# Optimization experiments

Measured on AMD Instinct MI355X. Metric: run time of the kernel, lower is better.

Reference implementation:

```python
import jax, jax.numpy as jnp
import numpy as np
import math

H, B, T = 4, 32, 1000
EPROJS, DUNITS, DK, DV = 1024, 1024, 512, 512
ACONV_CHANS, ACONV_FILTS = 100, 100
FILTS = [ACONV_FILTS * (h + 1) // H for h in range(H)]  # 25, 50, 75, 100


def setup_inputs() -> dict:
    key = jax.random.key(0)
    ks = jax.random.split(key, 16)
    s = 0.02  # small init to keep tanh unsaturated
    ap = jax.random.uniform(ks[3], (H, B, T), dtype=jnp.float32)
    ap = ap / ap.sum(-1, keepdims=True)  # previous attention weights (rows sum to 1)
    inp = {
        "enc_hs_pad": jax.random.normal(ks[0], (B, T, EPROJS), dtype=jnp.float32),
        "enc_hs_len": jnp.full((B,), T, dtype=jnp.int32),
        "dec_z": jax.random.normal(ks[1], (B, DUNITS), dtype=jnp.float32),
        "att_prev": ap,
        "Wq": jax.random.normal(ks[4], (H, DUNITS, DK), dtype=jnp.float32) * s,
        "bq": jnp.zeros((H, DK), dtype=jnp.float32),
        "Wk": jax.random.normal(ks[5], (H, EPROJS, DK), dtype=jnp.float32) * s,
        "Wv": jax.random.normal(ks[6], (H, EPROJS, DV), dtype=jnp.float32) * s,
        "g_w": jax.random.normal(ks[7], (H, DK), dtype=jnp.float32) * s,
        "g_b": jnp.zeros((H,), dtype=jnp.float32),
        "Watt": jax.random.normal(ks[8], (H, ACONV_CHANS, DK), dtype=jnp.float32) * s,
        "Wo": jax.random.normal(ks[9], (H * DV, EPROJS), dtype=jnp.float32) * s,
    }
    for h in range(H):
        inp[f"conv_w{h}"] = jax.random.normal(ks[10 + h], (ACONV_CHANS, 1, 2 * FILTS[h] + 1), dtype=jnp.float32) * s
    return inp


def _conv1d(x, w, f):
    # x: [B, T], w: [C, 1, K]; SAME padding like torch Conv2d(padding=(0, f)) -> [B, C, T]
    return jax.lax.conv_general_dilated(x[:, None, :], w, (1,), [(f, f)],
                                        dimension_numbers=("NCH", "OIH", "NCH"))


def reference(enc_hs_pad, enc_hs_len, dec_z, att_prev, Wq, bq, Wk, Wv, g_w, g_b,
              Watt, Wo, conv_w0, conv_w1, conv_w2, conv_w3):
    scaling = 1.0 / math.sqrt(DK)
    conv_ws = [conv_w0, conv_w1, conv_w2, conv_w3]
    # per-head K/V projections of encoder states: [H, B, T, dk/dv]
    k = jnp.einsum('btd,hde->hbte', enc_hs_pad, Wk)
    v = jnp.einsum('btd,hde->hbte', enc_hs_pad, Wv)
    # per-head query projection: [H, B, dk]
    q = jnp.einsum('bd,hde->hbe', dec_z, Wq) + bq[:, None, :]
    # location features: per-head conv (different filter widths) then linear -> [H, B, T, dk]
    att_conv = jnp.stack([_conv1d(att_prev[h], conv_ws[h], FILTS[h]).transpose(0, 2, 1)
                          for h in range(H)])  # [H, B, T, C]
    att_conv = jnp.einsum('hbtc,hce->hbte', att_conv, Watt)
    # energies via gvec: [H, B, T]
    e = jnp.einsum('hbte,he->hbt', jnp.tanh(k + att_conv + q[:, :, None, :]), g_w) + g_b[:, None, None]
    w = jax.nn.softmax(scaling * e, axis=-1)  # no length masking, as in the original
    # weighted sums per head, concatenated head-major: [B, H*dv]
    c = jnp.einsum('hbte,hbt->bhe', v, w).reshape(B, H * DV)
    out = c @ Wo  # [B, eprojs]
    return out, w
```

## Files before the change

### kernel.cpp

```cpp
#include <hip/hip_runtime.h>
#include <hip/hip_bf16.h>
#include <math.h>

#define Hh 4
#define Bb 32
#define Tt 1000
#define TP 1024
#define EPROJS_ 1024
#define DUNITS_ 1024
#define DKd 512
#define DVd 512
#define CC 100
#define KPAD 256
#define SCALING 0.04419417382415922f

typedef __attribute__((ext_vector_type(8))) short short8;
typedef __attribute__((ext_vector_type(4))) float floatx4;

__device__ __forceinline__ void async16(const void* g, void* l) {
    __builtin_amdgcn_global_load_lds(
        (const __attribute__((address_space(1))) unsigned int*)g,
        (__attribute__((address_space(3))) unsigned int*)l, 16, 0, 0);
}

__global__ __launch_bounds__(256) void enc_cvt_kernel(
    const float* __restrict__ enc, unsigned short* __restrict__ enc16)
{
    int t = blockIdx.x, b = blockIdx.y;
    int d = threadIdx.x * 4;
    float4 v = *(const float4*)(enc + ((size_t)(b * Tt + t)) * EPROJS_ + d);
    union { __hip_bfloat162 h2[2]; uint2 u; } u;
    u.h2[0] = __float22bfloat162_rn(make_float2(v.x, v.y));
    u.h2[1] = __float22bfloat162_rn(make_float2(v.z, v.w));
    *(uint2*)(enc16 + ((size_t)(b * TP + t)) * EPROJS_ + d) = u.u;
}

__global__ __launch_bounds__(256) void wkt_kernel(
    const float* __restrict__ Wk, unsigned short* __restrict__ Wkt)
{
    int et = blockIdx.x;
    int dt = blockIdx.y;
    int h  = blockIdx.z;
    __shared__ float tile[64][65];
    int tid = threadIdx.x;
    int r = tid >> 4, c4 = tid & 15;
    const float* src = Wk + ((size_t)(h * DUNITS_ + dt * 64)) * DKd + et * 64;
#pragma unroll
    for (int rr = 0; rr < 4; ++rr) {
        int row = r + rr * 16;
        *(float4*)&tile[row][c4 * 4] = *(const float4*)(src + (size_t)row * DKd + c4 * 4);
    }
    __syncthreads();
    unsigned short* dst = Wkt + ((size_t)(h * DKd + et * 64)) * EPROJS_ + dt * 64;
#pragma unroll
    for (int rr = 0; rr < 4; ++rr) {
        int el = r + rr * 16;
        union { __hip_bfloat162 h2[2]; uint2 u; } u;
        u.h2[0] = __float22bfloat162_rn(make_float2(tile[c4 * 4 + 0][el], tile[c4 * 4 + 1][el]));
        u.h2[1] = __float22bfloat162_rn(make_float2(tile[c4 * 4 + 2][el], tile[c4 * 4 + 3][el]));
        *(uint2*)(dst + (size_t)el * EPROJS_ + c4 * 4) = u.u;
    }
}

__global__ __launch_bounds__(256) void ww_kernel(
    const float* __restrict__ w0, const float* __restrict__ w1,
    const float* __restrict__ w2, const float* __restrict__ w3,
    const float* __restrict__ Watt, __hip_bfloat16* __restrict__ WWt)
{
    int k = blockIdx.x;
    int h = blockIdx.y;
    int f = 25 * (h + 1), Kh = 2 * f + 1;
    const float* cw = (h == 0) ? w0 : (h == 1) ? w1 : (h == 2) ? w2 : w3;
    int e = threadIdx.x;
    float acc0 = 0.f, acc1 = 0.f;
    if (k < Kh) {
        for (int c = 0; c < CC; ++c) {
            float wv = cw[c * Kh + k];
            acc0 += wv * Watt[(h * CC + c) * DKd + e];
            acc1 += wv * Watt[(h * CC + c) * DKd + e + 256];
        }
    }
    WWt[((size_t)(h * DKd + e)) * KPAD + k] = __float2bfloat16(acc0);
    WWt[((size_t)(h * DKd + e + 256)) * KPAD + k] = __float2bfloat16(acc1);
}

__global__ __launch_bounds__(256) void q_kernel(
    const float* __restrict__ dec_z, const float* __restrict__ Wq,
    float* __restrict__ q_buf)
{
    int et = blockIdx.x, kc = blockIdx.y, h = blockIdx.z;
    int d0 = kc * 64;
    __shared__ float zs[32][64];
    int tid = threadIdx.x;
    {
        int b = tid >> 3, dc = (tid & 7) * 8;
        const float* p = dec_z + (size_t)b * DUNITS_ + d0 + dc;
        *(float4*)&zs[b][dc] = *(const float4*)p;
        *(float4*)&zs[b][dc + 4] = *(const float4*)(p + 4);
    }
    __syncthreads();
    int e = et * 128 + (tid & 127);
    int dl0 = (tid >> 7) * 32;
    float wq[32];
#pragma unroll
    for (int dl = 0; dl < 32; ++dl)
        wq[dl] = Wq[((size_t)(h * DUNITS_ + d0 + dl0 + dl)) * DKd + e];
#pragma unroll
    for (int b = 0; b < 32; ++b) {
        float s = 0.f;
#pragma unroll
        for (int dl = 0; dl < 32; ++dl) s += zs[b][dl0 + dl] * wq[dl];
        atomicAdd(&q_buf[(h * Bb + b) * DKd + e], s);
    }
}

__global__ __launch_bounds__(256) void e_kernel(
    const unsigned short* __restrict__ enc16, const unsigned short* __restrict__ Wkt,
    const float* __restrict__ att_prev, const __hip_bfloat16* __restrict__ WWt,
    const float* __restrict__ q_buf, const float* __restrict__ bq,
    const float* __restrict__ g_w, float* __restrict__ e_buf)
{
    const int lin = blockIdx.x;
    const int xcd = lin & 7, pos = lin >> 3;
    const int b = (pos >> 7) * 8 + xcd;
    const int rem = pos & 127;
    const int h = rem >> 5;
    const int by = (rem & 31) >> 2;
    const int bx = rem & 3;
    const int t0 = by * 128, e0 = bx * 128;
    const int tid = threadIdx.x;
    const int lane = tid & 63, w = tid >> 6;
    const int wr = w >> 1, wc = w & 1;
    const int m = lane & 15, quad = lane >> 4;
    const int srow = tid >> 3;
    const int ko = (((tid & 7) ^ (srow & 7))) * 8;
    const int sw = m & 7;

    __shared__ __align__(16) short As[128 * 64];
    __shared__ __align__(16) short Bs[128 * 64];

    floatx4 acc[4][4];
#pragma unroll
    for (int i = 0; i < 4; ++i)
#pragma unroll
        for (int j = 0; j < 4; ++j) acc[i][j] = (floatx4){0.f, 0.f, 0.f, 0.f};

    const unsigned short* WkB = Wkt + ((size_t)(h * DKd + e0)) * EPROJS_;
    const unsigned short* encB = enc16 + ((size_t)(b * TP + t0)) * EPROJS_;
    char* AsDst = (char*)As + (tid & ~63) * 16;
    char* BsDst = (char*)Bs + (tid & ~63) * 16;

    for (int ch = 0; ch < 16; ++ch) {
        int d0 = ch * 64;
        __syncthreads();
#pragma unroll
        for (int it = 0; it < 4; ++it) {
            int r2 = it * 32 + srow;
            async16(encB + (size_t)r2 * EPROJS_ + d0 + ko, AsDst + it * 4096);
            async16(WkB + (size_t)r2 * EPROJS_ + d0 + ko, BsDst + it * 4096);
        }
        __syncthreads();
#pragma unroll
        for (int ks = 0; ks < 2; ++ks) {
            short8 af[4], bf[4];
#pragma unroll
            for (int i = 0; i < 4; ++i)
                af[i] = *(const short8*)&As[(wr * 64 + i * 16 + m) * 64 + (((ks << 2) + quad) ^ sw) * 8];
#pragma unroll
            for (int j = 0; j < 4; ++j)
                bf[j] = *(const short8*)&Bs[(wc * 64 + j * 16 + m) * 64 + (((ks << 2) + quad) ^ sw) * 8];
#pragma unroll
            for (int i = 0; i < 4; ++i)
#pragma unroll
                for (int j = 0; j < 4; ++j)
                    acc[i][j] = __builtin_amdgcn_mfma_f32_16x16x32_bf16(
                        af[i], bf[j], acc[i][j], 0, 0, 0);
        }
    }

    const int f = 25 * (h + 1);
    const int Kh = 2 * f + 1;
    const int nch2 = (Kh + 63) >> 6;
    const float* ab = att_prev + (size_t)(h * Bb + b) * Tt;
    const __hip_bfloat16* WWB = WWt + ((size_t)(h * DKd + e0)) * KPAD;
    for (int ch = 0; ch < nch2; ++ch) {
        int k0 = ch * 64;
        int ar = tid >> 1, half = tid & 1;
        int sbase = t0 + ar - f + k0 + half * 32;
        float v[32];
#pragma unroll
        for (int j2 = 0; j2 < 32; ++j2) {
            int s = sbase + j2;
            v[j2] = (s >= 0 && s < Tt) ? ab[s] : 0.f;
        }
        __syncthreads();
#pragma unroll
        for (int it = 0; it < 4; ++it) {
            int r2 = it * 32 + srow;
            async16(WWB + (size_t)r2 * KPAD + k0 + ko, BsDst + it * 4096);
        }
        union { short8 s[4]; __hip_bfloat162 hh[16]; } u;
#pragma unroll
        for (int j2 = 0; j2 < 16; ++j2)
            u.hh[j2] = __float22bfloat162_rn(make_float2(v[2 * j2], v[2 * j2 + 1]));
#pragma unroll
        for (int jj = 0; jj < 4; ++jj) {
            int phys = (half * 4 + jj) ^ (ar & 7);
            *(short8*)&As[ar * 64 + phys * 8] = u.s[jj];
        }
        __syncthreads();
#pragma unroll
        for (int ks = 0; ks < 2; ++ks) {
            short8 af[4], bf[4];
#pragma unroll
            for (int i = 0; i < 4; ++i)
                af[i] = *(const short8*)&As[(wr * 64 + i * 16 + m) * 64 + (((ks << 2) + quad) ^ sw) * 8];
#pragma unroll
            for (int j = 0; j < 4; ++j)
                bf[j] = *(const short8*)&Bs[(wc * 64 + j * 16 + m) * 64 + (((ks << 2) + quad) ^ sw) * 8];
#pragma unroll
            for (int i = 0; i < 4; ++i)
#pragma unroll
                for (int j = 0; j < 4; ++j)
                    acc[i][j] = __builtin_amdgcn_mfma_f32_16x16x32_bf16(
                        af[i], bf[j], acc[i][j], 0, 0, 0);
        }
    }

    const float* qrow = q_buf + (size_t)(h * Bb + b) * DKd;
    const float* bqrow = bq + h * DKd;
    const float* gwrow = g_w + h * DKd;
    float qv[4], gw[4];
#pragma unroll
    for (int j = 0; j < 4; ++j) {
        int e = e0 + wc * 64 + j * 16 + m;
        qv[j] = qrow[e] + bqrow[e];
        gw[j] = gwrow[e];
    }
    float* erow = e_buf + (size_t)(h * Bb + b) * Tt;
#pragma unroll
    for (int i = 0; i < 4; ++i) {
#pragma unroll
        for (int reg = 0; reg < 4; ++reg) {
            float s = 0.f;
#pragma unroll
            for (int j = 0; j < 4; ++j)
                s += tanhf(acc[i][j][reg] + qv[j]) * gw[j];
            s += __shfl_xor(s, 1);
            s += __shfl_xor(s, 2);
            s += __shfl_xor(s, 4);
            s += __shfl_xor(s, 8);
            int t = t0 + wr * 64 + i * 16 + quad * 4 + reg;
            if (m == 0 && t < Tt)
                atomicAdd(&erow[t], s);
        }
    }
}

__global__ __launch_bounds__(256) void softmax_kernel(
    const float* __restrict__ e_buf, float* __restrict__ wout)
{
    int rowid = blockIdx.x;
    const float* x = e_buf + rowid * Tt;
    float* y = wout + rowid * Tt;
    int tid = threadIdx.x;
    float v[4];
    float mx = -1e30f;
#pragma unroll
    for (int k = 0; k < 4; ++k) {
        int t = tid + k * 256;
        v[k] = (t < Tt) ? x[t] * SCALING : -1e30f;
        mx = fmaxf(mx, v[k]);
    }
    for (int off = 32; off >= 1; off >>= 1) mx = fmaxf(mx, __shfl_xor(mx, off));
    __shared__ float sm[4];
    __shared__ float ss[4];
    int wave = tid >> 6;
    if ((tid & 63) == 0) sm[wave] = mx;
    __syncthreads();
    mx = fmaxf(fmaxf(sm[0], sm[1]), fmaxf(sm[2], sm[3]));
    float s = 0.f;
#pragma unroll
    for (int k = 0; k < 4; ++k) {
        int t = tid + k * 256;
        v[k] = (t < Tt) ? __expf(v[k] - mx) : 0.f;
        s += v[k];
    }
    for (int off = 32; off >= 1; off >>= 1) s += __shfl_xor(s, off);
    if ((tid & 63) == 0) ss[wave] = s;
    __syncthreads();
    s = ss[0] + ss[1] + ss[2] + ss[3];
    float inv = 1.0f / s;
#pragma unroll
    for (int k = 0; k < 4; ++k) {
        int t = tid + k * 256;
        if (t < Tt) y[t] = v[k] * inv;
    }
}

__global__ __launch_bounds__(256) void ctx_kernel(
    const float* __restrict__ wout, const unsigned short* __restrict__ enc16,
    float* __restrict__ ctx)
{
    int dch = blockIdx.x;
    int b = blockIdx.y;
    int tq = blockIdx.z;
    int t0 = tq * 250;
    int tid = threadIdx.x;
    __shared__ float wl[4][252];
    __shared__ float red[8 * 4 * 128];
    for (int i = tid; i < 1000; i += 256) {
        int h = i / 250, tl = i - h * 250;
        wl[h][tl] = wout[(h * Bb + b) * Tt + t0 + tl];
    }
    __syncthreads();
    int g = tid >> 5, c = tid & 31;
    int d0 = dch * 128;
    float4 a[4];
#pragma unroll
    for (int h = 0; h < 4; ++h) a[h] = make_float4(0.f, 0.f, 0.f, 0.f);
    const unsigned short* encB = enc16 + (size_t)b * TP * EPROJS_ + d0 + c * 4;
    for (int t = t0 + g; t < t0 + 250; t += 8) {
        uint2 raw = *(const uint2*)(encB + (size_t)t * EPROJS_);
        float x0 = __uint_as_float(raw.x << 16);
        float x1 = __uint_as_float(raw.x & 0xffff0000u);
        float x2 = __uint_as_float(raw.y << 16);
        float x3 = __uint_as_float(raw.y & 0xffff0000u);
#pragma unroll
        for (int h = 0; h < 4; ++h) {
            float wv = wl[h][t - t0];
            a[h].x += wv * x0; a[h].y += wv * x1;
            a[h].z += wv * x2; a[h].w += wv * x3;
        }
    }
#pragma unroll
    for (int h = 0; h < 4; ++h)
        *(float4*)&red[((g * 4 + h) << 7) + c * 4] = a[h];
    __syncthreads();
    for (int i = tid; i < 512; i += 256) {
        int h = i >> 7, dd = i & 127;
        float ssum = 0.f;
#pragma unroll
        for (int g2 = 0; g2 < 8; ++g2) ssum += red[((g2 * 4 + h) << 7) + dd];
        atomicAdd(&ctx[(h * Bb + b) * EPROJS_ + d0 + dd], ssum);
    }
}

__global__ __launch_bounds__(256) void c_kernel(
    const float* __restrict__ ctx, const float* __restrict__ Wv,
    float* __restrict__ c_buf)
{
    int et = blockIdx.x, kc = blockIdx.y, h = blockIdx.z;
    int d0 = kc * 64;
    __shared__ float zs[32][64];
    int tid = threadIdx.x;
    {
        int b = tid >> 3, dc = (tid & 7) * 8;
        const float* p = ctx + ((size_t)(h * Bb + b)) * EPROJS_ + d0 + dc;
        *(float4*)&zs[b][dc] = *(const float4*)p;
        *(float4*)&zs[b][dc + 4] = *(const float4*)(p + 4);
    }
    __syncthreads();
    int e = et * 128 + (tid & 127);
    int dl0 = (tid >> 7) * 32;
    float wv[32];
#pragma unroll
    for (int dl = 0; dl < 32; ++dl)
        wv[dl] = Wv[((size_t)(h * EPROJS_ + d0 + dl0 + dl)) * DVd + e];
#pragma unroll
    for (int b = 0; b < 32; ++b) {
        float s = 0.f;
#pragma unroll
        for (int dl = 0; dl < 32; ++dl) s += zs[b][dl0 + dl] * wv[dl];
        atomicAdd(&c_buf[(h * Bb + b) * DVd + e], s);
    }
}

__global__ __launch_bounds__(256) void out_kernel(
    const float* __restrict__ c_buf, const float* __restrict__ Wo,
    float* __restrict__ outp)
{
    int ot = blockIdx.x;
    int kc = blockIdx.y;
    int k0 = kc * 64, o0 = ot * 128;
    __shared__ float cs[32][64];
    int tid = threadIdx.x;
    {
        int b = tid >> 3, k8 = (tid & 7) * 8;
        int h = k0 >> 9;
        const float* p = c_buf + ((size_t)(h * Bb + b)) * DVd + (k0 & 511) + k8;
        *(float4*)&cs[b][k8] = *(const float4*)p;
        *(float4*)&cs[b][k8 + 4] = *(const float4*)(p + 4);
    }
    __syncthreads();
    int o = o0 + (tid & 127);
    int kl0 = (tid >> 7) * 32;
    float wo[32];
#pragma unroll
    for (int kl = 0; kl < 32; ++kl)
        wo[kl] = Wo[((size_t)(k0 + kl0 + kl)) * EPROJS_ + o];
#pragma unroll
    for (int b = 0; b < 32; ++b) {
        float s = 0.f;
#pragma unroll
        for (int kl = 0; kl < 32; ++kl) s += cs[b][kl0 + kl] * wo[kl];
        atomicAdd(&outp[b * EPROJS_ + o], s);
    }
}

extern "C" void kernel_launch(void* const* d_in, const int* in_sizes, int n_in,
                              void* d_out, int out_size, void* d_ws, size_t ws_size,
                              hipStream_t stream) {
    const float* enc     = (const float*)d_in[0];
    const float* dec_z   = (const float*)d_in[2];
    const float* att_prev= (const float*)d_in[3];
    const float* Wq      = (const float*)d_in[4];
    const float* bq      = (const float*)d_in[5];
    const float* Wk      = (const float*)d_in[6];
    const float* Wv      = (const float*)d_in[7];
    const float* g_w     = (const float*)d_in[8];
    const float* Watt    = (const float*)d_in[10];
    const float* Wo      = (const float*)d_in[11];
    const float* cw0     = (const float*)d_in[12];
    const float* cw1     = (const float*)d_in[13];
    const float* cw2     = (const float*)d_in[14];
    const float* cw3     = (const float*)d_in[15];

    float* ws    = (float*)d_ws;
    float* q_buf = ws;
    float* e_buf = ws + 65536;
    float* c_buf = ws + 193536;
    float* ctx   = ws + 259072;
    unsigned short* enc16 = (unsigned short*)(ws + 390144);
    unsigned short* Wkt   = (unsigned short*)(ws + 17167360);
    __hip_bfloat16* WWt   = (__hip_bfloat16*)(ws + 18215936);
    float* outp  = (float*)d_out;
    float* wout  = outp + 32768;

    hipMemsetAsync(ws, 0, (size_t)390144 * sizeof(float), stream);
    hipMemsetAsync(d_out, 0, (size_t)32768 * sizeof(float), stream);

    enc_cvt_kernel<<<dim3(Tt, Bb), 256, 0, stream>>>(enc, enc16);
    wkt_kernel<<<dim3(8, 16, 4), 256, 0, stream>>>(Wk, Wkt);
    ww_kernel<<<dim3(KPAD, 4), 256, 0, stream>>>(cw0, cw1, cw2, cw3, Watt, WWt);
    q_kernel<<<dim3(4, 16, 4), 256, 0, stream>>>(dec_z, Wq, q_buf);
    e_kernel<<<4096, 256, 0, stream>>>(enc16, Wkt, att_prev, WWt,
                                       q_buf, bq, g_w, e_buf);
    softmax_kernel<<<128, 256, 0, stream>>>(e_buf, wout);
    ctx_kernel<<<dim3(8, 32, 4), 256, 0, stream>>>(wout, enc16, ctx);
    c_kernel<<<dim3(4, 16, 4), 256, 0, stream>>>(ctx, Wv, c_buf);
    out_kernel<<<dim3(8, 32), 256, 0, stream>>>(c_buf, Wo, outp);
}
```

Before: 568.1 us.

## Double-buffer K-projection LDS tiles and use fast tanh in energy epilogue

The main K-projection GEMM loop now uses two LDS buffers, prefetching the next 64-wide chunk with async global-to-LDS loads while MFMAs run on the current one. Explicit vmcnt waits and raw barriers replace the two __syncthreads per iteration. The libm tanhf in the energy epilogue is swapped for an exp plus reciprocal approximation with clamping. This doubles LDS use per block, which may lower occupancy, and the fast tanh is slightly less accurate.

```diff
diff --git a/kernel.cpp b/kernel.cpp
--- a/kernel.cpp
+++ b/kernel.cpp
@@ -21,6 +21,12 @@
     __builtin_amdgcn_global_load_lds(
         (const __attribute__((address_space(1))) unsigned int*)g,
         (__attribute__((address_space(3))) unsigned int*)l, 16, 0, 0);
+}
+
+__device__ __forceinline__ float fast_tanh(float x) {
+    float xc = fminf(fmaxf(x, -10.f), 10.f);
+    float t = __expf(2.f * xc);
+    return (t - 1.f) * __builtin_amdgcn_rcpf(t + 1.f);
 }
 
 __global__ __launch_bounds__(256) void enc_cvt_kernel(
@@ -136,8 +142,8 @@
     const int ko = (((tid & 7) ^ (srow & 7))) * 8;
     const int sw = m & 7;
 
-    __shared__ __align__(16) short As[128 * 64];
-    __shared__ __align__(16) short Bs[128 * 64];
+    __shared__ __align__(16) short As[2][128 * 64];
+    __shared__ __align__(16) short Bs[2][128 * 64];
 
     floatx4 acc[4][4];
 #pragma unroll
@@ -147,28 +153,40 @@
 
     const unsigned short* WkB = Wkt + ((size_t)(h * DKd + e0)) * EPROJS_;
     const unsigned short* encB = enc16 + ((size_t)(b * TP + t0)) * EPROJS_;
-    char* AsDst = (char*)As + (tid & ~63) * 16;
-    char* BsDst = (char*)Bs + (tid & ~63) * 16;
-
-    for (int ch = 0; ch < 16; ++ch) {
-        int d0 = ch * 64;
-        __syncthreads();
+
+    auto stage1 = [&](int chunk, int bi) {
+        const int d0 = chunk * 64;
+        char* ad = (char*)As[bi] + (tid & ~63) * 16;
+        char* bd = (char*)Bs[bi] + (tid & ~63) * 16;
 #pragma unroll
         for (int it = 0; it < 4; ++it) {
             int r2 = it * 32 + srow;
-            async16(encB + (size_t)r2 * EPROJS_ + d0 + ko, AsDst + it * 4096);
-            async16(WkB + (size_t)r2 * EPROJS_ + d0 + ko, BsDst + it * 4096);
-        }
-        __syncthreads();
+            async16(encB + (size_t)r2 * EPROJS_ + d0 + ko, ad + it * 4096);
+            async16(WkB + (size_t)r2 * EPROJS_ + d0 + ko, bd + it * 4096);
+        }
+    };
+
+    stage1(0, 0);
+    for (int ch = 0; ch < 16; ++ch) {
+        const int cur = ch & 1;
+        if (ch < 15) {
+            stage1(ch + 1, cur ^ 1);
+            asm volatile("s_waitcnt vmcnt(8)" ::: "memory");
+        } else {
+            asm volatile("s_waitcnt vmcnt(0)" ::: "memory");
+        }
+        __builtin_amdgcn_sched_barrier(0);
+        __builtin_amdgcn_s_barrier();
+        __builtin_amdgcn_sched_barrier(0);
 #pragma unroll
         for (int ks = 0; ks < 2; ++ks) {
             short8 af[4], bf[4];
 #pragma unroll
             for (int i = 0; i < 4; ++i)
-                af[i] = *(const short8*)&As[(wr * 64 + i * 16 + m) * 64 + (((ks << 2) + quad) ^ sw) * 8];
+                af[i] = *(const short8*)&As[cur][(wr * 64 + i * 16 + m) * 64 + (((ks << 2) + quad) ^ sw) * 8];
 #pragma unroll
             for (int j = 0; j < 4; ++j)
-                bf[j] = *(const short8*)&Bs[(wc * 64 + j * 16 + m) * 64 + (((ks << 2) + quad) ^ sw) * 8];
+                bf[j] = *(const short8*)&Bs[cur][(wc * 64 + j * 16 + m) * 64 + (((ks << 2) + quad) ^ sw) * 8];
 #pragma unroll
             for (int i = 0; i < 4; ++i)
 #pragma unroll
@@ -176,6 +194,9 @@
                     acc[i][j] = __builtin_amdgcn_mfma_f32_16x16x32_bf16(
                         af[i], bf[j], acc[i][j], 0, 0, 0);
         }
+        __builtin_amdgcn_sched_barrier(0);
+        __builtin_amdgcn_s_barrier();
+        __builtin_amdgcn_sched_barrier(0);
     }
 
     const int f = 25 * (h + 1);
@@ -183,6 +204,7 @@
     const int nch2 = (Kh + 63) >> 6;
     const float* ab = att_prev + (size_t)(h * Bb + b) * Tt;
     const __hip_bfloat16* WWB = WWt + ((size_t)(h * DKd + e0)) * KPAD;
+    char* BsDst0 = (char*)Bs[0] + (tid & ~63) * 16;
     for (int ch = 0; ch < nch2; ++ch) {
         int k0 = ch * 64;
         int ar = tid >> 1, half = tid & 1;
@@ -197,7 +219,7 @@
 #pragma unroll
         for (int it = 0; it < 4; ++it) {
             int r2 = it * 32 + srow;
-            async16(WWB + (size_t)r2 * KPAD + k0 + ko, BsDst + it * 4096);
+            async16(WWB + (size_t)r2 * KPAD + k0 + ko, BsDst0 + it * 4096);
         }
         union { short8 s[4]; __hip_bfloat162 hh[16]; } u;
 #pragma unroll
@@ -206,7 +228,7 @@
 #pragma unroll
         for (int jj = 0; jj < 4; ++jj) {
             int phys = (half * 4 + jj) ^ (ar & 7);
-            *(short8*)&As[ar * 64 + phys * 8] = u.s[jj];
+            *(short8*)&As[0][ar * 64 + phys * 8] = u.s[jj];
         }
         __syncthreads();
 #pragma unroll
@@ -214,10 +236,10 @@
             short8 af[4], bf[4];
 #pragma unroll
             for (int i = 0; i < 4; ++i)
-                af[i] = *(const short8*)&As[(wr * 64 + i * 16 + m) * 64 + (((ks << 2) + quad) ^ sw) * 8];
+                af[i] = *(const short8*)&As[0][(wr * 64 + i * 16 + m) * 64 + (((ks << 2) + quad) ^ sw) * 8];
 #pragma unroll
             for (int j = 0; j < 4; ++j)
-                bf[j] = *(const short8*)&Bs[(wc * 64 + j * 16 + m) * 64 + (((ks << 2) + quad) ^ sw) * 8];
+                bf[j] = *(const short8*)&Bs[0][(wc * 64 + j * 16 + m) * 64 + (((ks << 2) + quad) ^ sw) * 8];
 #pragma unroll
             for (int i = 0; i < 4; ++i)
 #pragma unroll
@@ -245,7 +267,7 @@
             float s = 0.f;
 #pragma unroll
             for (int j = 0; j < 4; ++j)
-                s += tanhf(acc[i][j][reg] + qv[j]) * gw[j];
+                s += fast_tanh(acc[i][j][reg] + qv[j]) * gw[j];
             s += __shfl_xor(s, 1);
             s += __shfl_xor(s, 2);
             s += __shfl_xor(s, 4);
```

Result: no change. 573.2 us (+0.9%).
